# Performance work log

Hardware: AMD Instinct MI355X
Metric: run time of the kernel (lower is better)

## Reference

```python
import jax, jax.numpy as jnp
import numpy as np

B, T, IN, H, OUT = 256, 2048, 182, 64, 2


def setup_inputs() -> dict:
    key = jax.random.key(0)
    ks = jax.random.split(key, 7)
    x = jax.random.normal(ks[0], (B, T, IN), dtype=jnp.float32)
    # equinox GRUCell params: weight_ih (3H, IN), weight_hh (3H, H), bias (3H,), bias_n (H,)
    s_ih = 1.0 / np.sqrt(IN)
    s_hh = 1.0 / np.sqrt(H)
    weight_ih = jax.random.uniform(ks[1], (3 * H, IN), jnp.float32, -s_ih, s_ih)
    weight_hh = jax.random.uniform(ks[2], (3 * H, H), jnp.float32, -s_hh, s_hh)
    bias = jax.random.uniform(ks[3], (3 * H,), jnp.float32, -s_hh, s_hh)
    bias_n = jax.random.uniform(ks[4], (H,), jnp.float32, -s_hh, s_hh)
    # readout: Linear(H, OUT, use_bias=False) plus explicit zero-init bias param
    w_out = jax.random.uniform(ks[5], (OUT, H), jnp.float32, -s_hh, s_hh)
    out_bias = jnp.zeros((OUT,), dtype=jnp.float32)
    return {"x": x, "weight_ih": weight_ih, "weight_hh": weight_hh,
            "bias": bias, "bias_n": bias_n, "w_out": w_out, "out_bias": out_bias}


def reference(x, weight_ih, weight_hh, bias, bias_n, w_out, out_bias):
    # Batched GRU scan over time (vmap of the per-trial lax.scan in the module).
    def step(h, xt):  # h: (B,H), xt: (B,IN)
        ig = xt @ weight_ih.T + bias          # (B, 3H)
        hg = h @ weight_hh.T                  # (B, 3H)
        ir, iz, inew = jnp.split(ig, 3, axis=-1)
        hr, hz, hn = jnp.split(hg, 3, axis=-1)
        r = jax.nn.sigmoid(ir + hr)           # reset gate
        z = jax.nn.sigmoid(iz + hz)           # update gate (equinox 'inp')
        n = jnp.tanh(inew + r * (hn + bias_n))
        return n + z * (h - n), None

    h0 = jnp.zeros((x.shape[0], weight_hh.shape[1]), dtype=x.dtype)
    hT, _ = jax.lax.scan(step, h0, jnp.swapaxes(x, 0, 1))  # scan over T
    return jax.nn.sigmoid(hT @ w_out.T + out_bias)          # (B, OUT)
```

## Files before the change

kernel.cpp:

```cpp
#include <hip/hip_runtime.h>
#include <hip/hip_fp16.h>
#include <cstdint>
#include <cstddef>

#define BB  256
#define TT  2048
#define KIN 182
#define HH  64
#define G3  192
#define CH  16
#define NC  (TT/CH)
#define IGS 196

#define NFRAG (12*6*64)
#define WS_NEEDED ((size_t)NFRAG*16)

typedef _Float16 half8 __attribute__((ext_vector_type(8)));
typedef _Float16 h2v   __attribute__((ext_vector_type(2)));
typedef float    f32x4 __attribute__((ext_vector_type(4)));
typedef float    v2f   __attribute__((ext_vector_type(2)));

static __device__ __forceinline__ float dot2(h2v a, h2v b, float c) {
#if __has_builtin(__builtin_amdgcn_fdot2)
    return __builtin_amdgcn_fdot2(a, b, c, false);
#else
    return c + (float)a[0] * (float)b[0] + (float)a[1] * (float)b[1];
#endif
}

__global__ void pack_wih(const float* __restrict__ wih, _Float16* __restrict__ wsB) {
    int idx = blockIdx.x * 256 + threadIdx.x;
    if (idx >= NFRAG) return;
    int lane = idx & 63;
    int kf   = (idx >> 6) % 6;
    int nt   = idx / (6 * 64);
    int col  = lane & 15, kq = lane >> 4;
    int n = nt * 16 + col;
    half8 t;
#pragma unroll
    for (int j = 0; j < 8; ++j) {
        int k = kf * 32 + kq * 8 + j;
        t[j] = (k < KIN) ? (_Float16)wih[n * KIN + k] : (_Float16)0.f;
    }
    *((half8*)wsB + idx) = t;
}

__global__ __launch_bounds__(128, 1) void gru_fused(
        const float* __restrict__ x,
        const _Float16* __restrict__ wsB,
        const float* __restrict__ whh,
        const float* __restrict__ bias,
        const float* __restrict__ bias_n,
        const float* __restrict__ wout,
        const float* __restrict__ outb,
        float* __restrict__ out)
{
    __shared__ float igb[2][CH][IGS];
    __shared__ __align__(16) _Float16 hs[HH];

    const int tid  = threadIdx.x;
    const int lane = tid & 63;
    const int wid  = tid >> 6;
    const int b    = blockIdx.x;

    if (wid == 1) {
        const int col = lane & 15;
        const int kq  = lane >> 4;
        float bv[12];
#pragma unroll
        for (int nt = 0; nt < 12; ++nt) bv[nt] = bias[nt * 16 + col];

        const float* xb    = x + (size_t)b * TT * KIN;
        const half8* bfrag = (const half8*)wsB + lane;

        auto produce = [&](int c, int buf) {
            const float* xr = xb + (size_t)(c * CH + col) * KIN + kq * 8;
            half8 af[6];
#pragma unroll
            for (int kf = 0; kf < 5; ++kf) {
                v2f a0 = *(const v2f*)(xr + kf * 32 + 0);
                v2f a1 = *(const v2f*)(xr + kf * 32 + 2);
                v2f a2 = *(const v2f*)(xr + kf * 32 + 4);
                v2f a3 = *(const v2f*)(xr + kf * 32 + 6);
                half8 t;
                t[0] = (_Float16)a0.x; t[1] = (_Float16)a0.y;
                t[2] = (_Float16)a1.x; t[3] = (_Float16)a1.y;
                t[4] = (_Float16)a2.x; t[5] = (_Float16)a2.y;
                t[6] = (_Float16)a3.x; t[7] = (_Float16)a3.y;
                af[kf] = t;
            }
            {
                v2f z2; z2.x = 0.f; z2.y = 0.f;
                half8 t;
#pragma unroll
                for (int j = 0; j < 4; ++j) {
                    int k = 160 + kq * 8 + 2 * j;
                    v2f a = (k <= 180) ? *(const v2f*)(xr + 160 + 2 * j) : z2;
                    t[2 * j]     = (_Float16)a.x;
                    t[2 * j + 1] = (_Float16)a.y;
                }
                af[5] = t;
            }
#pragma unroll
            for (int nt = 0; nt < 12; ++nt) {
                const half8* bp = bfrag + (size_t)nt * 6 * 64;
                half8 b0 = bp[0 * 64], b1 = bp[1 * 64], b2 = bp[2 * 64];
                half8 b3 = bp[3 * 64], b4 = bp[4 * 64], b5 = bp[5 * 64];
                f32x4 c4 = {bv[nt], bv[nt], bv[nt], bv[nt]};
                c4 = __builtin_amdgcn_mfma_f32_16x16x32_f16(af[0], b0, c4, 0, 0, 0);
                c4 = __builtin_amdgcn_mfma_f32_16x16x32_f16(af[1], b1, c4, 0, 0, 0);
                c4 = __builtin_amdgcn_mfma_f32_16x16x32_f16(af[2], b2, c4, 0, 0, 0);
                c4 = __builtin_amdgcn_mfma_f32_16x16x32_f16(af[3], b3, c4, 0, 0, 0);
                c4 = __builtin_amdgcn_mfma_f32_16x16x32_f16(af[4], b4, c4, 0, 0, 0);
                c4 = __builtin_amdgcn_mfma_f32_16x16x32_f16(af[5], b5, c4, 0, 0, 0);
                float* dst = &igb[buf][kq * 4][nt * 16 + col];
#pragma unroll
                for (int r = 0; r < 4; ++r) dst[r * IGS] = c4[r];
            }
        };

        produce(0, 0);
        __syncthreads();
        for (int c = 0; c < NC; ++c) {
            if (c + 1 < NC) produce(c + 1, (c + 1) & 1);
            __syncthreads();
        }
    } else {
        const int i = lane;
        h2v wr[32], wz[32], wn[32];
        {
            const v2f* pr = (const v2f*)(whh + (size_t)(0 * HH + i) * HH);
            const v2f* pz = (const v2f*)(whh + (size_t)(1 * HH + i) * HH);
            const v2f* pn = (const v2f*)(whh + (size_t)(2 * HH + i) * HH);
#pragma unroll
            for (int k = 0; k < 32; ++k) {
                v2f a = pr[k], c2 = pz[k], d2 = pn[k];
                h2v t;
                t[0] = (_Float16)a.x;  t[1] = (_Float16)a.y;  wr[k] = t;
                t[0] = (_Float16)c2.x; t[1] = (_Float16)c2.y; wz[k] = t;
                t[0] = (_Float16)d2.x; t[1] = (_Float16)d2.y; wn[k] = t;
            }
        }
        const float bn = bias_n[i];
        float h = 0.f;
        hs[i] = (_Float16)0.f;

        __syncthreads();

        for (int c = 0; c < NC; ++c) {
            const float* ig0 = &igb[c & 1][0][0];
            float pr_ = ig0[i], pz_ = ig0[64 + i], pn_ = ig0[128 + i];
#pragma unroll
            for (int lt = 0; lt < CH; ++lt) {
                const half8* hp = (const half8*)hs;
                float r0 = 0.f, r1 = 0.f, z0 = 0.f, z1 = 0.f, n0 = 0.f, n1 = 0.f;
#pragma unroll
                for (int q = 0; q < 8; ++q) {
                    half8 hv = hp[q];
                    h2v h0 = __builtin_shufflevector(hv, hv, 0, 1);
                    h2v h1 = __builtin_shufflevector(hv, hv, 2, 3);
                    h2v h2_ = __builtin_shufflevector(hv, hv, 4, 5);
                    h2v h3 = __builtin_shufflevector(hv, hv, 6, 7);
                    r0 = dot2(wr[4 * q + 0], h0, r0);
                    z0 = dot2(wz[4 * q + 0], h0, z0);
                    n0 = dot2(wn[4 * q + 0], h0, n0);
                    r1 = dot2(wr[4 * q + 1], h1, r1);
                    z1 = dot2(wz[4 * q + 1], h1, z1);
                    n1 = dot2(wn[4 * q + 1], h1, n1);
                    r0 = dot2(wr[4 * q + 2], h2_, r0);
                    z0 = dot2(wz[4 * q + 2], h2_, z0);
                    n0 = dot2(wn[4 * q + 2], h2_, n0);
                    r1 = dot2(wr[4 * q + 3], h3, r1);
                    z1 = dot2(wz[4 * q + 3], h3, z1);
                    n1 = dot2(wn[4 * q + 3], h3, n1);
                }
                float cr = pr_, cz = pz_, cn = pn_;
                if (lt != CH - 1) {
                    const float* p = ig0 + (lt + 1) * IGS;
                    pr_ = p[i]; pz_ = p[64 + i]; pn_ = p[128 + i];
                }
                float r  = __builtin_amdgcn_rcpf(1.f + __expf(-(cr + r0 + r1)));
                float z  = __builtin_amdgcn_rcpf(1.f + __expf(-(cz + z0 + z1)));
                float e  = __expf(2.f * (cn + r * ((n0 + n1) + bn)));
                float nn = 1.f - 2.f * __builtin_amdgcn_rcpf(e + 1.f);
                h = nn + z * (h - nn);
                __builtin_amdgcn_wave_barrier();
                hs[i] = (_Float16)h;
                __builtin_amdgcn_wave_barrier();
            }
            __syncthreads();
        }

        float s0 = wout[i] * h, s1 = wout[HH + i] * h;
#pragma unroll
        for (int off = 32; off > 0; off >>= 1) {
            s0 += __shfl_down(s0, off);
            s1 += __shfl_down(s1, off);
        }
        if (i == 0) {
            out[2 * b]     = __builtin_amdgcn_rcpf(1.f + __expf(-(s0 + outb[0])));
            out[2 * b + 1] = __builtin_amdgcn_rcpf(1.f + __expf(-(s1 + outb[1])));
        }
    }
}

extern "C" void kernel_launch(void* const* d_in, const int* in_sizes, int n_in,
                              void* d_out, int out_size, void* d_ws, size_t ws_size,
                              hipStream_t stream) {
    const float* x     = (const float*)d_in[0];
    const float* wih   = (const float*)d_in[1];
    const float* whh   = (const float*)d_in[2];
    const float* bias  = (const float*)d_in[3];
    const float* biasn = (const float*)d_in[4];
    const float* wout  = (const float*)d_in[5];
    const float* outb  = (const float*)d_in[6];
    float* out = (float*)d_out;

    if (ws_size < WS_NEEDED) {
        hipMemsetAsync(d_out, 0xFF, (size_t)out_size * sizeof(float), stream);
        return;
    }
    _Float16* wsB = (_Float16*)d_ws;

    pack_wih<<<(NFRAG + 255) / 256, 256, 0, stream>>>(wih, wsB);
    gru_fused<<<BB, 128, 0, stream>>>(x, wsB, whh, bias, biasn, wout, outb, out);
}
```

Measured before the change: 951.1 us.

## Interleave two batch sequences per block to hide recurrent step latency

Each block now processes two batch rows, with two producer waves computing input projections and one recurrent wave alternating GRU steps between the two sequences. The interleaving is meant to overlap the latency of one sequence's dependency chain (LDS round trip, dot products, transcendental ops) with the other's work. Hidden state is kept in registers, reloaded right after each write. The cost is half as many blocks, so only half the CUs are used, and twice the serial instruction work per recurrent wave.

New measurement: 1.554 ms. 63.4% more time.

```diff
diff --git a/kernel.cpp b/kernel.cpp
--- a/kernel.cpp
+++ b/kernel.cpp
@@ -11,6 +11,7 @@
 #define CH  16
 #define NC  (TT/CH)
 #define IGS 196
+#define NBLK (BB/2)
 
 #define NFRAG (12*6*64)
 #define WS_NEEDED ((size_t)NFRAG*16)
@@ -45,7 +46,7 @@
     *((half8*)wsB + idx) = t;
 }
 
-__global__ __launch_bounds__(128, 1) void gru_fused(
+__global__ __launch_bounds__(192, 1) void gru_fused(
         const float* __restrict__ x,
         const _Float16* __restrict__ wsB,
         const float* __restrict__ whh,
@@ -55,22 +56,23 @@
         const float* __restrict__ outb,
         float* __restrict__ out)
 {
-    __shared__ float igb[2][CH][IGS];
-    __shared__ __align__(16) _Float16 hs[HH];
+    __shared__ float igb[2][2][CH][IGS];
+    __shared__ __align__(16) _Float16 hs[2][HH];
 
     const int tid  = threadIdx.x;
     const int lane = tid & 63;
     const int wid  = tid >> 6;
-    const int b    = blockIdx.x;
-
-    if (wid == 1) {
+    const int b0   = 2 * blockIdx.x;
+
+    if (wid >= 1) {
+        const int seq = wid - 1;
         const int col = lane & 15;
         const int kq  = lane >> 4;
         float bv[12];
 #pragma unroll
         for (int nt = 0; nt < 12; ++nt) bv[nt] = bias[nt * 16 + col];
 
-        const float* xb    = x + (size_t)b * TT * KIN;
+        const float* xb    = x + (size_t)(b0 + seq) * TT * KIN;
         const half8* bfrag = (const half8*)wsB + lane;
 
         auto produce = [&](int c, int buf) {
@@ -104,16 +106,16 @@
 #pragma unroll
             for (int nt = 0; nt < 12; ++nt) {
                 const half8* bp = bfrag + (size_t)nt * 6 * 64;
-                half8 b0 = bp[0 * 64], b1 = bp[1 * 64], b2 = bp[2 * 64];
-                half8 b3 = bp[3 * 64], b4 = bp[4 * 64], b5 = bp[5 * 64];
+                half8 bq0 = bp[0 * 64], bq1 = bp[1 * 64], bq2 = bp[2 * 64];
+                half8 bq3 = bp[3 * 64], bq4 = bp[4 * 64], bq5 = bp[5 * 64];
                 f32x4 c4 = {bv[nt], bv[nt], bv[nt], bv[nt]};
-                c4 = __builtin_amdgcn_mfma_f32_16x16x32_f16(af[0], b0, c4, 0, 0, 0);
-                c4 = __builtin_amdgcn_mfma_f32_16x16x32_f16(af[1], b1, c4, 0, 0, 0);
-                c4 = __builtin_amdgcn_mfma_f32_16x16x32_f16(af[2], b2, c4, 0, 0, 0);
-                c4 = __builtin_amdgcn_mfma_f32_16x16x32_f16(af[3], b3, c4, 0, 0, 0);
-                c4 = __builtin_amdgcn_mfma_f32_16x16x32_f16(af[4], b4, c4, 0, 0, 0);
-                c4 = __builtin_amdgcn_mfma_f32_16x16x32_f16(af[5], b5, c4, 0, 0, 0);
-                float* dst = &igb[buf][kq * 4][nt * 16 + col];
+                c4 = __builtin_amdgcn_mfma_f32_16x16x32_f16(af[0], bq0, c4, 0, 0, 0);
+                c4 = __builtin_amdgcn_mfma_f32_16x16x32_f16(af[1], bq1, c4, 0, 0, 0);
+                c4 = __builtin_amdgcn_mfma_f32_16x16x32_f16(af[2], bq2, c4, 0, 0, 0);
+                c4 = __builtin_amdgcn_mfma_f32_16x16x32_f16(af[3], bq3, c4, 0, 0, 0);
+                c4 = __builtin_amdgcn_mfma_f32_16x16x32_f16(af[4], bq4, c4, 0, 0, 0);
+                c4 = __builtin_amdgcn_mfma_f32_16x16x32_f16(af[5], bq5, c4, 0, 0, 0);
+                float* dst = &igb[seq][buf][kq * 4][nt * 16 + col];
 #pragma unroll
                 for (int r = 0; r < 4; ++r) dst[r * IGS] = c4[r];
             }
@@ -142,64 +144,86 @@
             }
         }
         const float bn = bias_n[i];
-        float h = 0.f;
-        hs[i] = (_Float16)0.f;
+        float hA = 0.f, hB = 0.f;
+        hs[0][i] = (_Float16)0.f;
+        hs[1][i] = (_Float16)0.f;
 
         __syncthreads();
 
+        auto dostep = [&](half8* hv, float& h, _Float16* hsrow,
+                          float& cr, float& cz, float& cn, const float* ignext) {
+            float r0 = 0.f, r1 = 0.f, z0 = 0.f, z1 = 0.f, n0 = 0.f, n1 = 0.f;
+#pragma unroll
+            for (int q = 0; q < 8; ++q) {
+                half8 hv8 = hv[q];
+                h2v h0 = __builtin_shufflevector(hv8, hv8, 0, 1);
+                h2v h1 = __builtin_shufflevector(hv8, hv8, 2, 3);
+                h2v h2_ = __builtin_shufflevector(hv8, hv8, 4, 5);
+                h2v h3 = __builtin_shufflevector(hv8, hv8, 6, 7);
+                r0 = dot2(wr[4 * q + 0], h0, r0);
+                z0 = dot2(wz[4 * q + 0], h0, z0);
+                n0 = dot2(wn[4 * q + 0], h0, n0);
+                r1 = dot2(wr[4 * q + 1], h1, r1);
+                z1 = dot2(wz[4 * q + 1], h1, z1);
+                n1 = dot2(wn[4 * q + 1], h1, n1);
+                r0 = dot2(wr[4 * q + 2], h2_, r0);
+                z0 = dot2(wz[4 * q + 2], h2_, z0);
+                n0 = dot2(wn[4 * q + 2], h2_, n0);
+                r1 = dot2(wr[4 * q + 3], h3, r1);
+                z1 = dot2(wz[4 * q + 3], h3, z1);
+                n1 = dot2(wn[4 * q + 3], h3, n1);
+            }
+            float vr = cr, vz = cz, vn = cn;
+            cr = ignext[i]; cz = ignext[64 + i]; cn = ignext[128 + i];
+            float r  = __builtin_amdgcn_rcpf(1.f + __expf(-(vr + r0 + r1)));
+            float z  = __builtin_amdgcn_rcpf(1.f + __expf(-(vz + z0 + z1)));
+            float e  = __expf(2.f * (vn + r * ((n0 + n1) + bn)));
+            float nn = 1.f - 2.f * __builtin_amdgcn_rcpf(e + 1.f);
+            h = nn + z * (h - nn);
+            __builtin_amdgcn_wave_barrier();
+            hsrow[i] = (_Float16)h;
+            __builtin_amdgcn_wave_barrier();
+#pragma unroll
+            for (int q = 0; q < 8; ++q) hv[q] = ((const half8*)hsrow)[q];
+            __builtin_amdgcn_sched_group_barrier(0x100 , 8, 0);
+        };
+
+        half8 vA[8], vB[8];
+#pragma unroll
+        for (int q = 0; q < 8; ++q) {
+            vA[q] = ((const half8*)hs[0])[q];
+            vB[q] = ((const half8*)hs[1])[q];
+        }
+
         for (int c = 0; c < NC; ++c) {
-            const float* ig0 = &igb[c & 1][0][0];
-            float pr_ = ig0[i], pz_ = ig0[64 + i], pn_ = ig0[128 + i];
-#pragma unroll
+            const float* igA = &igb[0][c & 1][0][0];
+            const float* igB = &igb[1][c & 1][0][0];
+            float pAr = igA[i], pAz = igA[64 + i], pAn = igA[128 + i];
+            float pBr = igB[i], pBz = igB[64 + i], pBn = igB[128 + i];
+#pragma unroll 8
             for (int lt = 0; lt < CH; ++lt) {
-                const half8* hp = (const half8*)hs;
-                float r0 = 0.f, r1 = 0.f, z0 = 0.f, z1 = 0.f, n0 = 0.f, n1 = 0.f;
-#pragma unroll
-                for (int q = 0; q < 8; ++q) {
-                    half8 hv = hp[q];
-                    h2v h0 = __builtin_shufflevector(hv, hv, 0, 1);
-                    h2v h1 = __builtin_shufflevector(hv, hv, 2, 3);
-                    h2v h2_ = __builtin_shufflevector(hv, hv, 4, 5);
-                    h2v h3 = __builtin_shufflevector(hv, hv, 6, 7);
-                    r0 = dot2(wr[4 * q + 0], h0, r0);
-                    z0 = dot2(wz[4 * q + 0], h0, z0);
-                    n0 = dot2(wn[4 * q + 0], h0, n0);
-                    r1 = dot2(wr[4 * q + 1], h1, r1);
-                    z1 = dot2(wz[4 * q + 1], h1, z1);
-                    n1 = dot2(wn[4 * q + 1], h1, n1);
-                    r0 = dot2(wr[4 * q + 2], h2_, r0);
-                    z0 = dot2(wz[4 * q + 2], h2_, z0);
-                    n0 = dot2(wn[4 * q + 2], h2_, n0);
-                    r1 = dot2(wr[4 * q + 3], h3, r1);
-                    z1 = dot2(wz[4 * q + 3], h3, z1);
-                    n1 = dot2(wn[4 * q + 3], h3, n1);
-                }
-                float cr = pr_, cz = pz_, cn = pn_;
-                if (lt != CH - 1) {
-                    const float* p = ig0 + (lt + 1) * IGS;
-                    pr_ = p[i]; pz_ = p[64 + i]; pn_ = p[128 + i];
-                }
-                float r  = __builtin_amdgcn_rcpf(1.f + __expf(-(cr + r0 + r1)));
-                float z  = __builtin_amdgcn_rcpf(1.f + __expf(-(cz + z0 + z1)));
-                float e  = __expf(2.f * (cn + r * ((n0 + n1) + bn)));
-                float nn = 1.f - 2.f * __builtin_amdgcn_rcpf(e + 1.f);
-                h = nn + z * (h - nn);
-                __builtin_amdgcn_wave_barrier();
-                hs[i] = (_Float16)h;
-                __builtin_amdgcn_wave_barrier();
+                const float* nxA = igA + ((lt + 1) & 15) * IGS;
+                const float* nxB = igB + ((lt + 1) & 15) * IGS;
+                dostep(vA, hA, hs[0], pAr, pAz, pAn, nxA);
+                dostep(vB, hB, hs[1], pBr, pBz, pBn, nxB);
             }
             __syncthreads();
         }
 
-        float s0 = wout[i] * h, s1 = wout[HH + i] * h;
+        float s0A = wout[i] * hA, s1A = wout[HH + i] * hA;
+        float s0B = wout[i] * hB, s1B = wout[HH + i] * hB;
 #pragma unroll
         for (int off = 32; off > 0; off >>= 1) {
-            s0 += __shfl_down(s0, off);
-            s1 += __shfl_down(s1, off);
+            s0A += __shfl_down(s0A, off);
+            s1A += __shfl_down(s1A, off);
+            s0B += __shfl_down(s0B, off);
+            s1B += __shfl_down(s1B, off);
         }
         if (i == 0) {
-            out[2 * b]     = __builtin_amdgcn_rcpf(1.f + __expf(-(s0 + outb[0])));
-            out[2 * b + 1] = __builtin_amdgcn_rcpf(1.f + __expf(-(s1 + outb[1])));
+            out[2 * b0 + 0] = __builtin_amdgcn_rcpf(1.f + __expf(-(s0A + outb[0])));
+            out[2 * b0 + 1] = __builtin_amdgcn_rcpf(1.f + __expf(-(s1A + outb[1])));
+            out[2 * b0 + 2] = __builtin_amdgcn_rcpf(1.f + __expf(-(s0B + outb[0])));
+            out[2 * b0 + 3] = __builtin_amdgcn_rcpf(1.f + __expf(-(s1B + outb[1])));
         }
     }
 }
@@ -223,5 +247,5 @@
     _Float16* wsB = (_Float16*)d_ws;
 
     pack_wih<<<(NFRAG + 255) / 256, 256, 0, stream>>>(wih, wsB);
-    gru_fused<<<BB, 128, 0, stream>>>(x, wsB, whh, bias, biasn, wout, outb, out);
-}
+    gru_fused<<<NBLK, 192, 0, stream>>>(x, wsB, whh, bias, biasn, wout, outb, out);
+}
```
